# Optimization experiments

Measured on AMD Instinct MI355X. Metric: run time of the kernel, lower is better.

The kernel has to match this reference:

```python
import jax, jax.numpy as jnp
import numpy as np

N = 100000   # nodes
E = 1200000  # edges
IN = 128     # in_channels
H = 64       # hidden_channels


def setup_inputs() -> dict:
    key = jax.random.key(0)
    ks = jax.random.split(key, 8)
    x = jax.random.normal(ks[0], (N, IN), jnp.float32)
    edge_index = jax.random.randint(ks[1], (2, E), 0, N, dtype=jnp.int32)
    W_pre = jax.random.normal(ks[2], (IN, H), jnp.float32) * (1.0 / np.sqrt(IN))
    b_pre = jnp.zeros((H,), jnp.float32)
    W1 = jax.random.normal(ks[3], (H, H), jnp.float32) * (1.0 / np.sqrt(H))
    b1 = jnp.zeros((H,), jnp.float32)
    W2 = jax.random.normal(ks[4], (H, H), jnp.float32) * (1.0 / np.sqrt(H))
    b2 = jnp.zeros((H,), jnp.float32)
    return {"x": x, "edge_index": edge_index, "W_pre": W_pre, "b_pre": b_pre,
            "W1": W1, "b1": b1, "W2": W2, "b2": b2}


def _gcn_conv(x, src, dst, W, b, n):
    # PyG GCNConv: x' = D^{-1/2} (A + I) D^{-1/2} (x @ W) + b
    x = x @ W                                   # [N, H]
    deg = jax.ops.segment_sum(jnp.ones_like(dst, jnp.float32), dst, num_segments=n)
    dinv = jnp.where(deg > 0, jax.lax.rsqrt(jnp.maximum(deg, 1e-12)), 0.0)
    norm = dinv[src] * dinv[dst]                # [E+N]
    msg = x[src] * norm[:, None]                # gather + scale, [E+N, H]
    out = jax.ops.segment_sum(msg, dst, num_segments=n)  # scatter-add, [N, H]
    return out + b


def reference(x, edge_index, W_pre, b_pre, W1, b1, W2, b2):
    n = x.shape[0]
    loop = jnp.arange(n, dtype=edge_index.dtype)
    # add self-loops once (same structure both layers)
    src = jnp.concatenate([edge_index[0], loop])
    dst = jnp.concatenate([edge_index[1], loop])
    x = x @ W_pre + b_pre
    ori_x = x
    x = jax.nn.relu(_gcn_conv(x, src, dst, W1, b1, n))
    x = jax.nn.relu(_gcn_conv(x, src, dst, W2, b2, n))
    return (x, ori_x)
```

## Files before the change

### kernel.cpp

```cpp
#include <hip/hip_runtime.h>

#define H 64
#define NPB 128
#define BSHIFT 7
#define CAP 2048
#define CHUNK 4096
#define CPAD 16

typedef __attribute__((ext_vector_type(8))) short short8;
typedef __attribute__((ext_vector_type(4))) float floatx4;
typedef __attribute__((ext_vector_type(8))) unsigned short ushort8v;
typedef __attribute__((ext_vector_type(4))) unsigned short ushort4v;

static __device__ __forceinline__ unsigned short f2bf(float f) {
  union { float f; unsigned u; } x{f};
  unsigned r = x.u + 0x7fffu + ((x.u >> 16) & 1u);
  return (unsigned short)(r >> 16);
}
static __device__ __forceinline__ float bf2f(unsigned short u) {
  union { unsigned u; float f; } x{(unsigned)u << 16};
  return x.f;
}


__global__ __launch_bounds__(512) void bucket_scatter_kernel(const int* __restrict__ src,
                                                             const int* __restrict__ dst,
                                                             int* __restrict__ gcursor,
                                                             unsigned int* __restrict__ bpk,
                                                             int E, int NB) {
  __shared__ int cnt[1024];
  __shared__ int base[1024];
  int t = threadIdx.x;
  for (int i = t; i < NB; i += 512) cnt[i] = 0;
  __syncthreads();
  int cbase = blockIdx.x * CHUNK;
  int s[CHUNK / 512], d[CHUNK / 512];
#pragma unroll
  for (int j = 0; j < CHUNK / 512; ++j) {
    int e = cbase + j * 512 + t;
    s[j] = (e < E) ? src[e] : -1;
    d[j] = (e < E) ? dst[e] : -1;
    if (d[j] >= 0) atomicAdd(&cnt[d[j] >> BSHIFT], 1);
  }
  __syncthreads();
  for (int i = t; i < NB; i += 512)
    base[i] = cnt[i] ? (i * CAP + atomicAdd(&gcursor[i * CPAD], cnt[i])) : 0;
  __syncthreads();
  for (int i = t; i < NB; i += 512) cnt[i] = 0;
  __syncthreads();
#pragma unroll
  for (int j = 0; j < CHUNK / 512; ++j) {
    if (d[j] >= 0) {
      int b = d[j] >> BSHIFT;
      int r = atomicAdd(&cnt[b], 1);
      int slot = base[b] + r;
      if (slot < (b + 1) * CAP)
        bpk[slot] = ((unsigned)s[j] << BSHIFT) | (unsigned)(d[j] & (NPB - 1));
    }
  }
}


__global__ __launch_bounds__(256) void fine_sort_kernel(const unsigned int* __restrict__ bpk,
                                                        const int* __restrict__ gcursor,
                                                        int* __restrict__ csr,
                                                        unsigned int* __restrict__ rp,
                                                        float* __restrict__ dinv, int N) {
  __shared__ int cnt[NPB];
  __shared__ int woff[NPB];
  const int b = blockIdx.x;
  const int t = threadIdx.x;
  if (t < NPB) cnt[t] = 0;
  __syncthreads();
  const int beg = b * CAP;
  const int end = beg + min(gcursor[b * CPAD], CAP);
  for (int e = beg + t; e < end; e += 256)
    atomicAdd(&cnt[bpk[e] & (NPB - 1)], 1);
  __syncthreads();

  if (t < 64) {
    int lane = t;
    int c0 = cnt[lane];
    int c1 = cnt[64 + lane];
    int s0 = c0, s1 = c1;
#pragma unroll
    for (int off = 1; off < 64; off <<= 1) {
      int n0 = __shfl_up(s0, off, 64);
      int n1 = __shfl_up(s1, off, 64);
      if (lane >= off) { s0 += n0; s1 += n1; }
    }
    int tot0 = __shfl(s0, 63, 64);
    int o0 = s0 - c0;
    int o1 = tot0 + s1 - c1;
    woff[lane] = o0;
    woff[64 + lane] = o1;
    int node0 = b * NPB + lane;
    int node1 = node0 + 64;
    if (node0 < N) {
      rp[node0] = ((unsigned)(beg + o0) << 11) | (unsigned)min(c0, 2047);
      dinv[node0] = rsqrtf((float)(c0 + 1));
    }
    if (node1 < N) {
      rp[node1] = ((unsigned)(beg + o1) << 11) | (unsigned)min(c1, 2047);
      dinv[node1] = rsqrtf((float)(c1 + 1));
    }
  }
  __syncthreads();

  for (int e = beg + t; e < end; e += 256) {
    unsigned pk = bpk[e];
    int r = atomicAdd(&woff[pk & (NPB - 1)], 1);
    csr[beg + r] = (int)(pk >> BSHIFT);
  }
}


__global__ __launch_bounds__(256) void wprep_kernel(const float* __restrict__ Wpre,
                                                    const float* __restrict__ W1,
                                                    const float* __restrict__ W2,
                                                    unsigned short* __restrict__ frag) {
  int i = blockIdx.x * 256 + threadIdx.x;
  const float* W;
  int K, base;
  if (i < 8192) {
    W = Wpre; K = 128; base = 0;
  } else if (i < 12288) {
    W = W1; K = 64; base = 8192;
  } else if (i < 16384) {
    W = W2; K = 64; base = 12288;
  } else {
    return;
  }
  int s = i - base;
  int j = s & 7;
  int t = s >> 3;
  int l = t & 63;
  int t2 = t >> 6;
  int KB = K / 32;
  int kb = t2 % KB;
  int w = t2 / KB;
  int k = kb * 32 + ((l >> 4) & 3) * 8 + j;
  int n = w * 16 + (l & 15);
  frag[i] = f2bf(W[k * H + n]);
}


__global__ __launch_bounds__(256) void fused_gemm_kernel(
    const float* __restrict__ X, const unsigned short* __restrict__ Wfrag,
    const float* __restrict__ bpre, const float* __restrict__ dinv,
    float* __restrict__ ori, unsigned short* __restrict__ g, int N) {
  __shared__ __align__(16) unsigned short As[4 * 64 * 8];
  __shared__ __align__(16) unsigned short os[16 * 72];
  __shared__ float dinv_s[16];
  const int tid = threadIdx.x;
  const int w = tid >> 6;
  const int lane = tid & 63;
  const int row0 = blockIdx.x * 16;

  {
    int kb = tid >> 6;
    int l = tid & 63;
    int m = l & 15;
    int k0 = kb * 32 + (l >> 4) * 8;
    int r = row0 + m;
    ushort8v v = {0, 0, 0, 0, 0, 0, 0, 0};
    if (r < N) {
      const float* xp = &X[(size_t)r * 128 + k0];
      float4 a = *(const float4*)xp;
      float4 b = *(const float4*)(xp + 4);
      v = ushort8v{f2bf(a.x), f2bf(a.y), f2bf(a.z), f2bf(a.w),
                   f2bf(b.x), f2bf(b.y), f2bf(b.z), f2bf(b.w)};
    }
    *(ushort8v*)&As[(kb * 64 + l) * 8] = v;
  }
  if (tid < 16) dinv_s[tid] = (row0 + tid < N) ? dinv[row0 + tid] : 1.f;

  short8 bfragP[4], bfrag1[2];
  {
    const unsigned short* wf = &Wfrag[((size_t)(w * 4) * 64 + lane) * 8];
#pragma unroll
    for (int kb = 0; kb < 4; ++kb) bfragP[kb] = *(const short8*)&wf[kb * 512];
    const unsigned short* wf1 = &Wfrag[8192 + ((size_t)(w * 2) * 64 + lane) * 8];
#pragma unroll
    for (int kb = 0; kb < 2; ++kb) bfrag1[kb] = *(const short8*)&wf1[kb * 512];
  }
  __syncthreads();

  floatx4 accP = {0.f, 0.f, 0.f, 0.f};
#pragma unroll
  for (int kb = 0; kb < 4; ++kb) {
    short8 a = *(const short8*)&As[(kb * 64 + lane) * 8];
    accP = __builtin_amdgcn_mfma_f32_16x16x32_bf16(a, bfragP[kb], accP, 0, 0, 0);
  }

  const int c = w * 16 + (lane & 15);
  const int q = lane >> 4;
  {
    float bv = bpre[c];
#pragma unroll
    for (int r = 0; r < 4; ++r) {
      int m = q * 4 + r;
      int row = row0 + m;
      float v = accP[r] + bv;
      if (row < N) ori[(size_t)row * H + c] = v;
      os[m * 72 + c] = f2bf(v);
    }
  }
  __syncthreads();

  floatx4 acc2 = {0.f, 0.f, 0.f, 0.f};
#pragma unroll
  for (int kb = 0; kb < 2; ++kb) {
    short8 a = *(const short8*)&os[(lane & 15) * 72 + kb * 32 + (lane >> 4) * 8];
    acc2 = __builtin_amdgcn_mfma_f32_16x16x32_bf16(a, bfrag1[kb], acc2, 0, 0, 0);
  }
#pragma unroll
  for (int r = 0; r < 4; ++r) {
    int row = row0 + q * 4 + r;
    if (row < N) g[(size_t)row * H + c] = f2bf(acc2[r] * dinv_s[q * 4 + r]);
  }
}


__global__ __launch_bounds__(256) void mfma_gemm_kernel(
    const unsigned short* __restrict__ X, const unsigned short* __restrict__ Wfrag,
    const float* __restrict__ dinv, unsigned short* __restrict__ out, int N) {
  __shared__ __align__(16) unsigned short As[2 * 64 * 8];
  __shared__ float dinv_s[16];
  const int tid = threadIdx.x;
  const int w = tid >> 6;
  const int lane = tid & 63;
  const int row0 = blockIdx.x * 16;

  {
    int kb = tid >> 7;
    int hh = tid & 127;
    int l = hh >> 1;
    int j0 = (tid & 1) * 4;
    int m = l & 15;
    int k0 = kb * 32 + (l >> 4) * 8 + j0;
    int r = row0 + m;
    ushort4v v = {0, 0, 0, 0};
    if (r < N) v = *(const ushort4v*)&X[(size_t)r * 64 + k0];
    *(ushort4v*)&As[(kb * 64 + l) * 8 + j0] = v;
  }
  if (tid < 16) dinv_s[tid] = (row0 + tid < N) ? dinv[row0 + tid] : 1.f;

  short8 bfrag[2];
  const unsigned short* wf = &Wfrag[((size_t)(w * 2) * 64 + lane) * 8];
#pragma unroll
  for (int kb = 0; kb < 2; ++kb) bfrag[kb] = *(const short8*)&wf[kb * 512];

  __syncthreads();

  floatx4 acc = {0.f, 0.f, 0.f, 0.f};
#pragma unroll
  for (int kb = 0; kb < 2; ++kb) {
    short8 a = *(const short8*)&As[(kb * 64 + lane) * 8];
    acc = __builtin_amdgcn_mfma_f32_16x16x32_bf16(a, bfrag[kb], acc, 0, 0, 0);
  }

  int c = w * 16 + (lane & 15);
  int q = lane >> 4;
#pragma unroll
  for (int r = 0; r < 4; ++r) {
    int row = row0 + q * 4 + r;
    if (row < N) out[(size_t)row * H + c] = f2bf(acc[r] * dinv_s[q * 4 + r]);
  }
}


template <typename OutT>
__global__ __launch_bounds__(256) void gather_kernel(const unsigned short* __restrict__ g,
                                                     const unsigned int* __restrict__ rp,
                                                     const int* __restrict__ csr,
                                                     const float* __restrict__ dinv,
                                                     const float* __restrict__ bias,
                                                     OutT* __restrict__ out, int N) {
  int node = (blockIdx.x * 256 + threadIdx.x) >> 6;
  int c = threadIdx.x & 63;
  if (node >= N) return;

  float acc = bf2f(g[(size_t)node * H + c]);
  unsigned v0 = rp[node];
  int beg = (int)(v0 >> 11);
  int end = beg + (int)(v0 & 2047);
  for (int base = beg; base < end; base += 64) {
    int m = min(64, end - base);
    int myidx = (c < m) ? csr[base + c] : node;
    int nb8 = (m + 7) >> 3;
    for (int b8 = 0; b8 < nb8; ++b8) {
      int j0 = b8 * 8;
      float v[8];
#pragma unroll
      for (int u = 0; u < 8; ++u) {
        int sidx = __builtin_amdgcn_readlane(myidx, j0 + u);
        const unsigned short* rowp = g + (size_t)sidx * H;
        v[u] = bf2f(rowp[c]);
      }
#pragma unroll
      for (int u = 0; u < 8; ++u)
        if (j0 + u < m) acc += v[u];
    }
  }
  float v = fmaxf(fmaf(dinv[node], acc, bias[c]), 0.f);
  if constexpr (sizeof(OutT) == 2)
    out[(size_t)node * H + c] = (OutT)f2bf(v);
  else
    out[(size_t)node * H + c] = v;
}


extern "C" void kernel_launch(void* const* d_in, const int* in_sizes, int n_in,
                              void* d_out, int out_size, void* d_ws, size_t ws_size,
                              hipStream_t stream) {
  const float* x = (const float*)d_in[0];
  const int* ei = (const int*)d_in[1];
  const float* W_pre = (const float*)d_in[2];
  const float* b_pre = (const float*)d_in[3];
  const float* W1 = (const float*)d_in[4];
  const float* b1 = (const float*)d_in[5];
  const float* W2 = (const float*)d_in[6];
  const float* b2 = (const float*)d_in[7];

  const int IN = 128;
  const int N = in_sizes[0] / IN;
  const int E = in_sizes[1] / 2;
  const int* src = ei;
  const int* dst = ei + E;
  const int NB = (N + NPB - 1) / NPB;

  float* out = (float*)d_out;
  float* ori = out + (size_t)N * H;

  char* p = (char*)d_ws;
  auto take = [&](size_t bytes) {
    char* q = p;
    p += (bytes + 255) & ~(size_t)255;
    return q;
  };
  int* gcursor = (int*)take(1024 * CPAD * 4);
  unsigned int* rp = (unsigned int*)take((size_t)N * 4);
  float* dinv = (float*)take((size_t)N * 4);
  unsigned int* bpk = (unsigned int*)take((size_t)NB * CAP * 4);
  int* csr = (int*)take((size_t)NB * CAP * 4);
  unsigned short* g = (unsigned short*)take((size_t)N * H * 2);
  unsigned short* x1b = (unsigned short*)take((size_t)N * H * 2);
  unsigned short* wfrag = (unsigned short*)take(16384 * 2);

  hipMemsetAsync(gcursor, 0, (size_t)NB * CPAD * 4, stream);

  int eb = (E + CHUNK - 1) / CHUNK;
  bucket_scatter_kernel<<<eb, 512, 0, stream>>>(src, dst, gcursor, bpk, E, NB);
  fine_sort_kernel<<<NB, 256, 0, stream>>>(bpk, gcursor, csr, rp, dinv, N);
  wprep_kernel<<<64, 256, 0, stream>>>(W_pre, W1, W2, wfrag);

  int gb = (N + 15) / 16;
  int nb = (N + 3) / 4;

  fused_gemm_kernel<<<gb, 256, 0, stream>>>(x, wfrag, b_pre, dinv, ori, g, N);
  gather_kernel<unsigned short><<<nb, 256, 0, stream>>>(g, rp, csr, dinv, b1, x1b, N);
  mfma_gemm_kernel<<<gb, 256, 0, stream>>>(x1b, wfrag + 12288, dinv, g, N);
  gather_kernel<float><<<nb, 256, 0, stream>>>(g, rp, csr, dinv, b2, out, N);
}
```

Before: 246.8 us.

## Fuse layer-1 gather with layer-2 MFMA GEMM into one kernel

Result: no change. 243.2 us (-1.4%).

```diff
diff --git a/kernel.cpp b/kernel.cpp
--- a/kernel.cpp
+++ b/kernel.cpp
@@ -222,61 +222,78 @@
 }
 
 
-__global__ __launch_bounds__(256) void mfma_gemm_kernel(
-    const unsigned short* __restrict__ X, const unsigned short* __restrict__ Wfrag,
-    const float* __restrict__ dinv, unsigned short* __restrict__ out, int N) {
-  __shared__ __align__(16) unsigned short As[2 * 64 * 8];
+__global__ __launch_bounds__(1024) void gather_fused_kernel(
+    const unsigned short* __restrict__ g, const unsigned int* __restrict__ rp,
+    const int* __restrict__ csr, const float* __restrict__ dinv,
+    const float* __restrict__ bias, const unsigned short* __restrict__ w2frag,
+    unsigned short* __restrict__ out, int N) {
+  __shared__ __align__(16) unsigned short os[16 * 72];
   __shared__ float dinv_s[16];
   const int tid = threadIdx.x;
   const int w = tid >> 6;
   const int lane = tid & 63;
-  const int row0 = blockIdx.x * 16;
-
-  {
-    int kb = tid >> 7;
-    int hh = tid & 127;
-    int l = hh >> 1;
-    int j0 = (tid & 1) * 4;
-    int m = l & 15;
-    int k0 = kb * 32 + (l >> 4) * 8 + j0;
-    int r = row0 + m;
-    ushort4v v = {0, 0, 0, 0};
-    if (r < N) v = *(const ushort4v*)&X[(size_t)r * 64 + k0];
-    *(ushort4v*)&As[(kb * 64 + l) * 8 + j0] = v;
-  }
-  if (tid < 16) dinv_s[tid] = (row0 + tid < N) ? dinv[row0 + tid] : 1.f;
-
-  short8 bfrag[2];
-  const unsigned short* wf = &Wfrag[((size_t)(w * 2) * 64 + lane) * 8];
-#pragma unroll
-  for (int kb = 0; kb < 2; ++kb) bfrag[kb] = *(const short8*)&wf[kb * 512];
-
-  __syncthreads();
-
-  floatx4 acc = {0.f, 0.f, 0.f, 0.f};
-#pragma unroll
-  for (int kb = 0; kb < 2; ++kb) {
-    short8 a = *(const short8*)&As[(kb * 64 + lane) * 8];
-    acc = __builtin_amdgcn_mfma_f32_16x16x32_bf16(a, bfrag[kb], acc, 0, 0, 0);
-  }
-
-  int c = w * 16 + (lane & 15);
-  int q = lane >> 4;
-#pragma unroll
-  for (int r = 0; r < 4; ++r) {
-    int row = row0 + q * 4 + r;
-    if (row < N) out[(size_t)row * H + c] = f2bf(acc[r] * dinv_s[q * 4 + r]);
-  }
-}
-
-
-template <typename OutT>
+  const int node0 = blockIdx.x * 16;
+  const int node = node0 + w;
+
+  if (tid < 16) dinv_s[tid] = (node0 + tid < N) ? dinv[node0 + tid] : 1.f;
+
+  float x1 = 0.f;
+  if (node < N) {
+    float acc = bf2f(g[(size_t)node * H + lane]);
+    unsigned v0 = rp[node];
+    int beg = (int)(v0 >> 11);
+    int end = beg + (int)(v0 & 2047);
+    for (int base = beg; base < end; base += 64) {
+      int m = min(64, end - base);
+      int myidx = (lane < m) ? csr[base + lane] : node;
+      int nb8 = (m + 7) >> 3;
+      for (int b8 = 0; b8 < nb8; ++b8) {
+        int j0 = b8 * 8;
+        float v[8];
+#pragma unroll
+        for (int u = 0; u < 8; ++u) {
+          int sidx = __builtin_amdgcn_readlane(myidx, j0 + u);
+          const unsigned short* rowp = g + (size_t)sidx * H;
+          v[u] = bf2f(rowp[lane]);
+        }
+#pragma unroll
+        for (int u = 0; u < 8; ++u)
+          if (j0 + u < m) acc += v[u];
+      }
+    }
+    x1 = fmaxf(fmaf(dinv[node], acc, bias[lane]), 0.f);
+  }
+  os[w * 72 + lane] = f2bf(x1);
+  __syncthreads();
+
+  if (w < 4) {
+    short8 bfrag[2];
+#pragma unroll
+    for (int kb = 0; kb < 2; ++kb)
+      bfrag[kb] = *(const short8*)&w2frag[((size_t)(w * 2 + kb) * 64 + lane) * 8];
+    floatx4 acc2 = {0.f, 0.f, 0.f, 0.f};
+#pragma unroll
+    for (int kb = 0; kb < 2; ++kb) {
+      short8 a = *(const short8*)&os[(lane & 15) * 72 + kb * 32 + (lane >> 4) * 8];
+      acc2 = __builtin_amdgcn_mfma_f32_16x16x32_bf16(a, bfrag[kb], acc2, 0, 0, 0);
+    }
+    const int c = w * 16 + (lane & 15);
+    const int q = lane >> 4;
+#pragma unroll
+    for (int r = 0; r < 4; ++r) {
+      int row = node0 + q * 4 + r;
+      if (row < N) out[(size_t)row * H + c] = f2bf(acc2[r] * dinv_s[q * 4 + r]);
+    }
+  }
+}
+
+
 __global__ __launch_bounds__(256) void gather_kernel(const unsigned short* __restrict__ g,
                                                      const unsigned int* __restrict__ rp,
                                                      const int* __restrict__ csr,
                                                      const float* __restrict__ dinv,
                                                      const float* __restrict__ bias,
-                                                     OutT* __restrict__ out, int N) {
+                                                     float* __restrict__ out, int N) {
   int node = (blockIdx.x * 256 + threadIdx.x) >> 6;
   int c = threadIdx.x & 63;
   if (node >= N) return;
@@ -303,11 +320,7 @@
         if (j0 + u < m) acc += v[u];
     }
   }
-  float v = fmaxf(fmaf(dinv[node], acc, bias[c]), 0.f);
-  if constexpr (sizeof(OutT) == 2)
-    out[(size_t)node * H + c] = (OutT)f2bf(v);
-  else
-    out[(size_t)node * H + c] = v;
+  out[(size_t)node * H + c] = fmaxf(fmaf(dinv[node], acc, bias[c]), 0.f);
 }
 
 
@@ -344,8 +357,8 @@
   float* dinv = (float*)take((size_t)N * 4);
   unsigned int* bpk = (unsigned int*)take((size_t)NB * CAP * 4);
   int* csr = (int*)take((size_t)NB * CAP * 4);
-  unsigned short* g = (unsigned short*)take((size_t)N * H * 2);
-  unsigned short* x1b = (unsigned short*)take((size_t)N * H * 2);
+  unsigned short* g1 = (unsigned short*)take((size_t)N * H * 2);
+  unsigned short* g2 = (unsigned short*)take((size_t)N * H * 2);
   unsigned short* wfrag = (unsigned short*)take(16384 * 2);
 
   hipMemsetAsync(gcursor, 0, (size_t)NB * CPAD * 4, stream);
@@ -358,8 +371,8 @@
   int gb = (N + 15) / 16;
   int nb = (N + 3) / 4;
 
-  fused_gemm_kernel<<<gb, 256, 0, stream>>>(x, wfrag, b_pre, dinv, ori, g, N);
-  gather_kernel<unsigned short><<<nb, 256, 0, stream>>>(g, rp, csr, dinv, b1, x1b, N);
-  mfma_gemm_kernel<<<gb, 256, 0, stream>>>(x1b, wfrag + 12288, dinv, g, N);
-  gather_kernel<float><<<nb, 256, 0, stream>>>(g, rp, csr, dinv, b2, out, N);
-}
+  fused_gemm_kernel<<<gb, 256, 0, stream>>>(x, wfrag, b_pre, dinv, ori, g1, N);
+  gather_fused_kernel<<<gb, 1024, 0, stream>>>(g1, rp, csr, dinv, b1,
+                                               wfrag + 12288, g2, N);
+  gather_kernel<<<nb, 256, 0, stream>>>(g2, rp, csr, dinv, b2, out, N);
+}
```
